# Optimization experiments

Measured on AMD Instinct MI355X. Metric: run time of the kernel, lower is better.

## Reference

```python
import jax, jax.numpy as jnp
import numpy as np


def _conv(x, w, b, pad):
    y = jax.lax.conv_general_dilated(
        x, w, window_strides=(1, 1), padding=[(pad, pad), (pad, pad)],
        dimension_numbers=('NCHW', 'OIHW', 'NCHW'))
    return y + b[None, :, None, None]


def _grid_sample(img, gxn, gyn):
    # img [N,C,H,W]; gxn,gyn [N,H,W] normalized coords.
    # Matches torch grid_sample(mode='bilinear', padding_mode='zeros', align_corners=False).
    N, C, H, W = img.shape
    ix = ((gxn + 1.0) * W - 1.0) * 0.5
    iy = ((gyn + 1.0) * H - 1.0) * 0.5
    ix0 = jnp.floor(ix); iy0 = jnp.floor(iy)
    ix1 = ix0 + 1.0; iy1 = iy0 + 1.0
    wx1 = ix - ix0; wy1 = iy - iy0
    wx0 = 1.0 - wx1; wy0 = 1.0 - wy1
    bidx = jnp.arange(N)[:, None, None]

    def gather(yy, xx):
        valid = (xx >= 0) & (xx < W) & (yy >= 0) & (yy < H)
        xc = jnp.clip(xx, 0, W - 1).astype(jnp.int32)
        yc = jnp.clip(yy, 0, H - 1).astype(jnp.int32)
        v = img[bidx, :, yc, xc]  # [N,H,W,C]
        return jnp.where(valid[..., None], v, jnp.zeros((), img.dtype))

    out = (gather(iy0, ix0) * (wy0 * wx0)[..., None]
           + gather(iy0, ix1) * (wy0 * wx1)[..., None]
           + gather(iy1, ix0) * (wy1 * wx0)[..., None]
           + gather(iy1, ix1) * (wy1 * wx1)[..., None])
    return jnp.transpose(out, (0, 3, 1, 2))  # [N,C,H,W]


def reference(inputs, state, i2h_w, i2h_b, i2f_w, i2f_b, h2f_w, h2f_b,
              flows_w, flows_b, wrap_w, wrap_b):
    B, T, Cin, H, W = inputs.shape
    hid = state.shape[1]
    L = flows_w.shape[0] // 2

    # input-to-hidden for all timesteps at once (as in the torch code)
    i2h = _conv(inputs.reshape(B * T, Cin, H, W), i2h_w, i2h_b, 1)
    i2h = i2h.reshape(B, T, 3 * hid, H, W)
    r_i, u_i, n_i = jnp.split(i2h, 3, axis=2)

    gx, gy = jnp.meshgrid(jnp.arange(W, dtype=inputs.dtype),
                          jnp.arange(H, dtype=inputs.dtype))  # each [H,W]

    def step(h, xs):
        x_t, r_t, u_t, n_t = xs
        f = jnp.tanh(_conv(x_t, i2f_w, i2f_b, 2) + _conv(h, h2f_w, h2f_b, 2))
        flows = _conv(f, flows_w, flows_b, 2).reshape(B, L, 2, H, W)
        # vgrid = grid + (-flow), then normalize by 2*v/size - 1
        vx = gx[None, None] - flows[:, :, 0]
        vy = gy[None, None] - flows[:, :, 1]
        gxn = 2.0 * vx / W - 1.0
        gyn = 2.0 * vy / H - 1.0
        img = jnp.broadcast_to(h[:, None], (B, L, hid, H, W)).reshape(B * L, hid, H, W)
        warped = _grid_sample(img, gxn.reshape(B * L, H, W), gyn.reshape(B * L, H, W))
        warped = warped.reshape(B, L * hid, H, W)
        h2h = _conv(warped, wrap_w, wrap_b, 0)
        r_h, u_h, n_h = jnp.split(h2h, 3, axis=1)
        r = jax.nn.sigmoid(r_t + r_h)
        u = jax.nn.sigmoid(u_t + u_h)
        n = jax.nn.sigmoid(n_t + r * n_h)  # note: sigmoid, faithful to source
        h_new = (1.0 - u) * n + u * h
        return h_new, h_new

    xs = (jnp.swapaxes(inputs, 0, 1),
          jnp.swapaxes(r_i, 0, 1),
          jnp.swapaxes(u_i, 0, 1),
          jnp.swapaxes(n_i, 0, 1))
    h_last, outs = jax.lax.scan(step, state, xs)
    outputs = jnp.swapaxes(outs, 0, 1)  # [B,T,hid,H,W]
    return outputs, h_last


def setup_inputs() -> dict:
    key = jax.random.key(0)
    ks = jax.random.split(key, 8)
    B, T, Cin, H, W = 4, 10, 8, 96, 96
    hid, L = 64, 13

    def w(k, shape):
        fan_in = int(np.prod(shape[1:]))
        return jax.random.normal(k, shape, jnp.float32) * (1.0 / np.sqrt(fan_in))

    return {
        'inputs': jax.random.normal(ks[0], (B, T, Cin, H, W), jnp.float32),
        'state': jnp.zeros((B, hid, H, W), jnp.float32),
        'i2h_w': w(ks[1], (3 * hid, Cin, 3, 3)), 'i2h_b': jnp.zeros((3 * hid,), jnp.float32),
        'i2f_w': w(ks[2], (32, Cin, 5, 5)), 'i2f_b': jnp.zeros((32,), jnp.float32),
        'h2f_w': w(ks[3], (32, hid, 5, 5)), 'h2f_b': jnp.zeros((32,), jnp.float32),
        'flows_w': w(ks[4], (2 * L, 32, 5, 5)), 'flows_b': jnp.zeros((2 * L,), jnp.float32),
        'wrap_w': w(ks[5], (3 * hid, hid * L, 1, 1)), 'wrap_b': jnp.zeros((3 * hid,), jnp.float32),
    }
```

## Files before the change

kernel.cpp:

```cpp
#include <hip/hip_runtime.h>
#include <math.h>

#define HW 9216

typedef __attribute__((ext_vector_type(8))) short short8;
typedef __attribute__((ext_vector_type(4))) short short4v;
typedef __attribute__((ext_vector_type(4))) float float4v;

__device__ __forceinline__ float sigmoidf_(float x) { return 1.0f / (1.0f + expf(-x)); }

__device__ __forceinline__ short bf16rne(float f) {
  unsigned u = __builtin_bit_cast(unsigned, f);
  unsigned r = (u + 0x7FFFu + ((u >> 16) & 1u)) >> 16;
  return (short)r;
}
__device__ __forceinline__ float bf2f(short s) {
  return __builtin_bit_cast(float, ((unsigned)(unsigned short)s) << 16);
}

__global__ __launch_bounds__(256) void k_wconv(const float* __restrict__ w,
                                               short* __restrict__ o)
{
  int i = blockIdx.x * 256 + threadIdx.x;
  if (i >= 192 * 832) return;
  int n = i / 832, k = i % 832;
  int l = k >> 6, c = k & 63;
  o[((size_t)l * 192 + n) * 64 + c] = bf16rne(w[i]);
}

__global__ __launch_bounds__(256) void k_pack(
    const float* __restrict__ wh, const float* __restrict__ wi,
    const float* __restrict__ flw, const float* __restrict__ wih,
    short* __restrict__ whK, short* __restrict__ wiK, short* __restrict__ flK,
    short* __restrict__ i2hK)
{
  int i = blockIdx.x * 256 + threadIdx.x;
  if (i < 51200) {
    int t = i / 2048, rem = i % 2048;
    int o = rem / 64, c = rem % 64;
    whK[i] = bf16rne(wh[((size_t)(o * 64 + c)) * 25 + t]);
  } else if (i < 58368) {
    int j = i - 51200;
    int g = j / 1024, rem = j % 1024;
    int o = rem / 32, k = rem % 32;
    int q = k / 8, ch = k % 8;
    int tap = g * 4 + q;
    wiK[j] = (tap < 25) ? bf16rne(wi[((size_t)(o * 8 + ch)) * 25 + tap]) : (short)0;
  } else if (i < 83968) {
    int j = i - 58368;
    int t = j / 1024, rem = j % 1024;
    int o = rem / 32, c = rem % 32;
    flK[j] = (o < 26) ? bf16rne(flw[((size_t)(o * 32 + c)) * 25 + t]) : (short)0;
  } else {
    int j = i - 83968;
    int g = j / 6144, rem = j % 6144;
    int n = rem / 32, k = rem % 32;
    int q = k / 8, ch = k % 8;
    int tap = g * 4 + q;
    i2hK[j] = (tap < 9) ? bf16rne(wih[((size_t)(n * 8 + ch)) * 9 + tap]) : (short)0;
  }
}

__global__ __launch_bounds__(256) void k_h2bf(const float* __restrict__ st,
                                              short* __restrict__ hbf)
{
  const int tid = threadIdx.x;
  const int pp = tid & 63, cg = tid >> 6;
  const int b = blockIdx.y;
  const int p = blockIdx.x * 64 + pp;
  short s[16];
  #pragma unroll
  for (int k = 0; k < 16; ++k)
    s[k] = bf16rne(st[((size_t)b * 64 + cg * 16 + k) * HW + p]);
  short* dst = hbf + ((size_t)b * HW + p) * 64 + cg * 16;
  *(short8*)dst = *(short8*)&s[0];
  *(short8*)(dst + 8) = *(short8*)&s[8];
}

__global__ __launch_bounds__(256) void k_x2bf(const float* __restrict__ inp,
                                              short* __restrict__ xbf)
{
  const int p  = blockIdx.x * 256 + threadIdx.x;
  const int bt = blockIdx.y;
  short s[8];
  #pragma unroll
  for (int ci = 0; ci < 8; ++ci)
    s[ci] = bf16rne(inp[((size_t)bt * 8 + ci) * HW + p]);
  *(short8*)(xbf + ((size_t)bt * HW + p) * 8) = *(short8*)s;
}

__global__ __launch_bounds__(256) void k_i2h(
    const short* __restrict__ xbf, int t_off,
    const short* __restrict__ wK, const float* __restrict__ bias,
    short* __restrict__ out)
{
  const int tid  = threadIdx.x;
  const int lane = tid & 63;
  const int w    = tid >> 6;
  const int ml = lane & 15, qd = lane >> 4;
  const int zz = blockIdx.y;
  const int t = (zz >> 2) + t_off, b = zz & 3;
  const int pw0 = blockIdx.x * 128 + w * 32;
  const short* xb = xbf + ((size_t)(b * 10 + t)) * HW * 8;

  short8 afr[2][3];
  #pragma unroll
  for (int s = 0; s < 2; ++s) {
    int px0 = pw0 + s * 16;
    int y0 = px0 / 96, xc0 = px0 % 96;
    #pragma unroll
    for (int g = 0; g < 3; ++g) {
      int tap = g * 4 + qd;
      int dy = tap / 3 - 1;
      int dx = tap % 3 - 1;
      int yy = y0 + dy, xx = xc0 + ml + dx;
      bool v = (tap < 9) && (yy >= 0) && (yy < 96) && (xx >= 0) && (xx < 96);
      short8 a = {};
      if (v) a = *(const short8*)(xb + (size_t)(px0 + ml + dy * 96 + dx) * 8);
      afr[s][g] = a;
    }
  }

  float4v acc[2][12];
  #pragma unroll
  for (int s = 0; s < 2; ++s)
    #pragma unroll
    for (int j = 0; j < 12; ++j)
      #pragma unroll
      for (int r = 0; r < 4; ++r) acc[s][j][r] = 0.0f;

  #pragma unroll
  for (int j = 0; j < 12; ++j) {
    #pragma unroll
    for (int g = 0; g < 3; ++g) {
      short8 bf = *(const short8*)(wK + ((size_t)(g * 192 + j * 16 + ml)) * 32 + qd * 8);
      acc[0][j] = __builtin_amdgcn_mfma_f32_16x16x32_bf16(afr[0][g], bf, acc[0][j], 0, 0, 0);
      acc[1][j] = __builtin_amdgcn_mfma_f32_16x16x32_bf16(afr[1][g], bf, acc[1][j], 0, 0, 0);
    }
  }

  #pragma unroll
  for (int j = 0; j < 12; ++j) {
    float bv = bias[j * 16 + ml];
    #pragma unroll
    for (int s = 0; s < 2; ++s) {
      short4v o4;
      #pragma unroll
      for (int r = 0; r < 4; ++r) o4[r] = bf16rne(acc[s][j][r] + bv);
      *(short4v*)(out + ((size_t)(zz * 192 + j * 16 + ml)) * HW
                      + pw0 + s * 16 + qd * 4) = o4;
    }
  }
}

__global__ __launch_bounds__(256) void k_f(
    const short* __restrict__ xbf, int t,
    const short* __restrict__ hbf,
    const short* __restrict__ whK,
    const short* __restrict__ wiK,
    const float* __restrict__ bi, const float* __restrict__ bh,
    short* __restrict__ fbf)
{
  const int tid = threadIdx.x;
  const int lane = tid & 63;
  const int w = tid >> 6;
  const int ml = lane & 15, qd = lane >> 4;
  const int b = blockIdx.y;
  const int px0 = blockIdx.x * 64 + w * 16;
  const int y0 = px0 / 96, xc0 = px0 % 96;
  const int xcol = xc0 + ml;
  const int px = px0 + ml;
  const short* hb = hbf + (size_t)b * HW * 64;
  const short* xb = xbf + ((size_t)(b * 10 + t)) * HW * 8;

  float4v acc0 = {0.f, 0.f, 0.f, 0.f};
  float4v acc1 = {0.f, 0.f, 0.f, 0.f};

  #pragma unroll
  for (int ky = 0; ky < 5; ++ky) {
    int yy = y0 + ky - 2;
    if (yy < 0 || yy >= 96) continue;
    #pragma unroll
    for (int kx = 0; kx < 5; ++kx) {
      int xx = xcol + kx - 2;
      bool cv = (xx >= 0) && (xx < 96);
      int off = (ky - 2) * 96 + (kx - 2);
      const short* ap = hb + (size_t)(px + off) * 64 + qd * 8;
      short8 a0 = {}, a1 = {};
      if (cv) { a0 = *(const short8*)ap; a1 = *(const short8*)(ap + 32); }
      int tap = ky * 5 + kx;
      const short* bp = whK + ((size_t)tap * 32 + ml) * 64 + qd * 8;
      short8 b00 = *(const short8*)bp;
      short8 b01 = *(const short8*)(bp + 32);
      short8 b10 = *(const short8*)(bp + 16 * 64);
      short8 b11 = *(const short8*)(bp + 16 * 64 + 32);
      acc0 = __builtin_amdgcn_mfma_f32_16x16x32_bf16(a0, b00, acc0, 0, 0, 0);
      acc0 = __builtin_amdgcn_mfma_f32_16x16x32_bf16(a1, b01, acc0, 0, 0, 0);
      acc1 = __builtin_amdgcn_mfma_f32_16x16x32_bf16(a0, b10, acc1, 0, 0, 0);
      acc1 = __builtin_amdgcn_mfma_f32_16x16x32_bf16(a1, b11, acc1, 0, 0, 0);
    }
  }

  #pragma unroll
  for (int g = 0; g < 7; ++g) {
    int tap = g * 4 + qd;
    int dy = tap / 5 - 2;
    int dx = tap - (dy + 2) * 5 - 2;
    int yy = y0 + dy, xx = xcol + dx;
    bool v = (tap < 25) && (yy >= 0) && (yy < 96) && (xx >= 0) && (xx < 96);
    short8 a = {};
    if (v) a = *(const short8*)(xb + (size_t)(px + dy * 96 + dx) * 8);
    const short* bp = wiK + ((size_t)g * 32 + ml) * 32 + qd * 8;
    short8 b0 = *(const short8*)bp;
    short8 b1 = *(const short8*)(bp + 16 * 32);
    acc0 = __builtin_amdgcn_mfma_f32_16x16x32_bf16(a, b0, acc0, 0, 0, 0);
    acc1 = __builtin_amdgcn_mfma_f32_16x16x32_bf16(a, b1, acc1, 0, 0, 0);
  }

  short* fo = fbf + (size_t)b * HW * 32;
  #pragma unroll
  for (int i = 0; i < 2; ++i) {
    int o = i * 16 + ml;
    float bias = bi[o] + bh[o];
    float4v a = i ? acc1 : acc0;
    #pragma unroll
    for (int r = 0; r < 4; ++r) {
      int p2 = px0 + qd * 4 + r;
      fo[(size_t)p2 * 32 + o] = bf16rne(tanhf(a[r] + bias));
    }
  }
}

__global__ __launch_bounds__(256) void k_flows(
    const short* __restrict__ fbf,
    const short* __restrict__ flK,
    const float* __restrict__ bias,
    float* __restrict__ fls)
{
  const int tid = threadIdx.x;
  const int lane = tid & 63;
  const int w = tid >> 6;
  const int ml = lane & 15, qd = lane >> 4;
  const int b = blockIdx.y;
  const int px0 = blockIdx.x * 64 + w * 16;
  const int y0 = px0 / 96, xc0 = px0 % 96;
  const int xcol = xc0 + ml;
  const int px = px0 + ml;
  const short* fb = fbf + (size_t)b * HW * 32;

  float4v acc0 = {0.f, 0.f, 0.f, 0.f};
  float4v acc1 = {0.f, 0.f, 0.f, 0.f};

  #pragma unroll
  for (int ky = 0; ky < 5; ++ky) {
    int yy = y0 + ky - 2;
    if (yy < 0 || yy >= 96) continue;
    #pragma unroll
    for (int kx = 0; kx < 5; ++kx) {
      int xx = xcol + kx - 2;
      bool cv = (xx >= 0) && (xx < 96);
      int off = (ky - 2) * 96 + (kx - 2);
      short8 a = {};
      if (cv) a = *(const short8*)(fb + (size_t)(px + off) * 32 + qd * 8);
      int tap = ky * 5 + kx;
      const short* bp = flK + ((size_t)tap * 32 + ml) * 32 + qd * 8;
      short8 b0 = *(const short8*)bp;
      short8 b1 = *(const short8*)(bp + 16 * 32);
      acc0 = __builtin_amdgcn_mfma_f32_16x16x32_bf16(a, b0, acc0, 0, 0, 0);
      acc1 = __builtin_amdgcn_mfma_f32_16x16x32_bf16(a, b1, acc1, 0, 0, 0);
    }
  }

  float* fo = fls + (size_t)b * 26 * HW;
  #pragma unroll
  for (int i = 0; i < 2; ++i) {
    int o = i * 16 + ml;
    if (o < 26) {
      float bv = bias[o];
      float4v a = i ? acc1 : acc0;
      #pragma unroll
      for (int r = 0; r < 4; ++r)
        fo[(size_t)o * HW + px0 + qd * 4 + r] = a[r] + bv;
    }
  }
}

__global__ __launch_bounds__(256) void k_fused(
    const float* __restrict__ fls,
    const float* __restrict__ hbase, long long hstr,
    const short* __restrict__ hbf_in,
    const short* __restrict__ i2h,
    const short* __restrict__ wbf,
    const float* __restrict__ wb,
    float* __restrict__ outb, long long ostr,
    short* __restrict__ hbf_out,
    float* __restrict__ lastb)
{
  __shared__ __align__(16) char smem_raw[49920];
  short* lds_w = (short*)smem_raw;
  short* lds_v = lds_w + 192 * 72;
  float* lds_h = (float*)smem_raw;
  short* hpack = (short*)smem_raw;

  const int tid = threadIdx.x;
  const int pp  = tid & 63;
  const int cg  = tid >> 6;
  const int ii  = blockIdx.x;
  const int xcd = ii & 7;
  const int b   = xcd >> 1;
  const int tile = ((ii >> 3) << 1) | (xcd & 1);
  const int p   = tile * 64 + pp;
  const int ypix = p / 96, xpix = p % 96;
  const float* hb  = hbase + (size_t)b * hstr;
  const short* hvp = hbf_in + ((size_t)b * HW) * 64 + cg * 16;
  const float* flb = fls + (size_t)b * 26 * HW;
  const int ml = pp & 15;
  const int qd = pp >> 4;

  float4v acc[3][4];
  #pragma unroll
  for (int i = 0; i < 3; ++i)
    #pragma unroll
    for (int j = 0; j < 4; ++j)
      #pragma unroll
      for (int r = 0; r < 4; ++r) acc[i][j][r] = 0.0f;

  for (int l = 0; l < 13; ++l) {
    __syncthreads();
    {
      const short* wsrc = wbf + (size_t)l * 192 * 64;
      #pragma unroll
      for (int it = 0; it < 6; ++it) {
        int idx = tid + it * 256;
        int n = idx >> 3, c8 = (idx & 7) * 8;
        short8 v = *(const short8*)(wsrc + n * 64 + c8);
        *(short8*)(lds_w + n * 72 + c8) = v;
      }
    }
    float fx = flb[(size_t)(2 * l) * HW + p];
    float fy = flb[(size_t)(2 * l + 1) * HW + p];
    float vx = (float)xpix - fx;
    float vy = (float)ypix - fy;
    float gxn = 2.0f * vx / 96.0f - 1.0f;
    float gyn = 2.0f * vy / 96.0f - 1.0f;
    float ix = ((gxn + 1.0f) * 96.0f - 1.0f) * 0.5f;
    float iy = ((gyn + 1.0f) * 96.0f - 1.0f) * 0.5f;
    float x0f = floorf(ix), y0f = floorf(iy);
    float wx1 = ix - x0f, wy1 = iy - y0f;
    float wx0 = 1.0f - wx1, wy0 = 1.0f - wy1;
    int x0 = (int)x0f, y0 = (int)y0f;
    bool vx0 = (x0 >= 0) && (x0 < 96);
    bool vx1 = (x0 + 1 >= 0) && (x0 + 1 < 96);
    bool vy0g = (y0 >= 0) && (y0 < 96);
    bool vy1g = (y0 + 1 >= 0) && (y0 + 1 < 96);
    int o00 = (vx0 && vy0g) ? (y0 * 96 + x0)           : -1;
    int o01 = (vx1 && vy0g) ? (y0 * 96 + x0 + 1)       : -1;
    int o10 = (vx0 && vy1g) ? ((y0 + 1) * 96 + x0)     : -1;
    int o11 = (vx1 && vy1g) ? ((y0 + 1) * 96 + x0 + 1) : -1;
    float w00 = wy0 * wx0, w01 = wy0 * wx1, w10 = wy1 * wx0, w11 = wy1 * wx1;

    float sum[16];
    #pragma unroll
    for (int k = 0; k < 16; ++k) sum[k] = 0.0f;
    #define TAP_(off, wgt)                                            \
      if ((off) >= 0) {                                               \
        const short* tp = hvp + (size_t)(off) * 64;                   \
        short8 u0 = *(const short8*)tp;                               \
        short8 u1 = *(const short8*)(tp + 8);                         \
        _Pragma("unroll")                                             \
        for (int k = 0; k < 8; ++k) {                                 \
          sum[k]     += (wgt) * bf2f(u0[k]);                          \
          sum[k + 8] += (wgt) * bf2f(u1[k]);                          \
        }                                                             \
      }
    TAP_(o00, w00) TAP_(o01, w01) TAP_(o10, w10) TAP_(o11, w11)
    #undef TAP_
    short vv[16];
    #pragma unroll
    for (int k = 0; k < 16; ++k) vv[k] = bf16rne(sum[k]);
    *(short8*)(lds_v + pp * 72 + cg * 16)     = *(short8*)&vv[0];
    *(short8*)(lds_v + pp * 72 + cg * 16 + 8) = *(short8*)&vv[8];
    __syncthreads();

    #pragma unroll
    for (int ks = 0; ks < 2; ++ks) {
      short8 af[3], bfr[4];
      #pragma unroll
      for (int i = 0; i < 3; ++i)
        af[i] = *(const short8*)(lds_w + (48 * cg + i * 16 + ml) * 72 + ks * 32 + qd * 8);
      #pragma unroll
      for (int j = 0; j < 4; ++j)
        bfr[j] = *(const short8*)(lds_v + (j * 16 + ml) * 72 + ks * 32 + qd * 8);
      #pragma unroll
      for (int i = 0; i < 3; ++i)
        #pragma unroll
        for (int j = 0; j < 4; ++j)
          acc[i][j] = __builtin_amdgcn_mfma_f32_16x16x32_bf16(af[i], bfr[j], acc[i][j], 0, 0, 0);
    }
  }

  __syncthreads();
  #pragma unroll
  for (int i = 0; i < 3; ++i)
    #pragma unroll
    for (int j = 0; j < 4; ++j)
      #pragma unroll
      for (int r = 0; r < 4; ++r) {
        int ch = 48 * cg + i * 16 + qd * 4 + r;
        int px = j * 16 + ml;
        lds_h[ch * 65 + px] = acc[i][j][r];
      }
  __syncthreads();

  const short* i2hb = i2h + (size_t)b * 192 * HW + p;
  float* ob = outb + (size_t)b * ostr;
  float hnv[16];
  #pragma unroll
  for (int k = 0; k < 16; ++k) {
    int cch = cg + k * 4;
    float rh = lds_h[cch * 65 + pp] + wb[cch];
    float uh = lds_h[(64 + cch) * 65 + pp] + wb[64 + cch];
    float nh = lds_h[(128 + cch) * 65 + pp] + wb[128 + cch];
    float rt = bf2f(i2hb[(size_t)cch * HW]);
    float ut = bf2f(i2hb[(size_t)(64 + cch) * HW]);
    float nt = bf2f(i2hb[(size_t)(128 + cch) * HW]);
    float rr = sigmoidf_(rt + rh);
    float uu = sigmoidf_(ut + uh);
    float nn = sigmoidf_(nt + rr * nh);
    float hp = hb[(size_t)cch * HW + p];
    float hn = (1.0f - uu) * nn + uu * hp;
    ob[(size_t)cch * HW + p] = hn;
    if (lastb) lastb[((size_t)b * 64 + cch) * HW + p] = hn;
    hnv[k] = hn;
  }

  __syncthreads();
  #pragma unroll
  for (int k = 0; k < 16; ++k)
    hpack[pp * 80 + cg + 4 * k] = bf16rne(hnv[k]);
  __syncthreads();
  {
    int px = tid >> 2, g = tid & 3;
    short8 a0 = *(short8*)(hpack + px * 80 + g * 16);
    short8 a1 = *(short8*)(hpack + px * 80 + g * 16 + 8);
    short* dst = hbf_out + ((size_t)b * HW + tile * 64 + px) * 64 + g * 16;
    *(short8*)dst = a0;
    *(short8*)(dst + 8) = a1;
  }
}

extern "C" void kernel_launch(void* const* d_in, const int* in_sizes, int n_in,
                              void* d_out, int out_size, void* d_ws, size_t ws_size,
                              hipStream_t stream)
{
  const float* inp   = (const float*)d_in[0];
  const float* state = (const float*)d_in[1];
  const float* i2h_w = (const float*)d_in[2];
  const float* i2h_b = (const float*)d_in[3];
  const float* i2f_w = (const float*)d_in[4];
  const float* i2f_b = (const float*)d_in[5];
  const float* h2f_w = (const float*)d_in[6];
  const float* h2f_b = (const float*)d_in[7];
  const float* fl_w  = (const float*)d_in[8];
  const float* fl_b  = (const float*)d_in[9];
  const float* wr_w  = (const float*)d_in[10];
  const float* wr_b  = (const float*)d_in[11];
  float* out = (float*)d_out;
  float* ws  = (float*)d_ws;

  const long long F_I2HB1 = 3538944;
  const long long F_FBF   = 589824;
  const long long F_FLS   = 958464;
  const long long F_HB    = 1179648;
  const long long F_XBF   = 1474560;
  const long long F_WBF   = 79872;
  const long long F_WHK   = 25600;
  const long long F_WIK   = 3584;
  const long long F_FLK   = 12800;
  const long long F_I2HK  = 9216;
  const long long OB      = (long long)10 * 64 * HW;

  const long long fixed = F_FBF + F_FLS + 2 * F_HB + F_XBF + F_WBF
                        + F_WHK + F_WIK + F_FLK + F_I2HK;
  bool batched = ws_size >= (size_t)(10 * F_I2HB1 + fixed) * 4ULL;
  long long i2h_fl = batched ? 10 * F_I2HB1 : F_I2HB1;

  short* ws_i2h = (short*)ws;
  float* fwp    = ws + i2h_fl;
  float* ws_fbf_f = fwp;              fwp += F_FBF;
  float* ws_fls   = fwp;              fwp += F_FLS;
  float* hbfA_f   = fwp;              fwp += F_HB;
  float* hbfB_f   = fwp;              fwp += F_HB;
  float* xbf_f    = fwp;              fwp += F_XBF;
  float* wbf_f    = fwp;              fwp += F_WBF;
  float* whK_f    = fwp;              fwp += F_WHK;
  float* wiK_f    = fwp;              fwp += F_WIK;
  float* flK_f    = fwp;              fwp += F_FLK;
  float* i2hK_f   = fwp;
  short* ws_fbf  = (short*)ws_fbf_f;
  short* hbfA    = (short*)hbfA_f;
  short* hbfB    = (short*)hbfB_f;
  short* ws_xbf  = (short*)xbf_f;
  short* ws_wbf  = (short*)wbf_f;
  short* ws_whK  = (short*)whK_f;
  short* ws_wiK  = (short*)wiK_f;
  short* ws_flK  = (short*)flK_f;
  short* ws_i2hK = (short*)i2hK_f;

  k_wconv<<<dim3(624), 256, 0, stream>>>(wr_w, ws_wbf);
  k_pack<<<dim3(400), 256, 0, stream>>>(h2f_w, i2f_w, fl_w, i2h_w,
                                        ws_whK, ws_wiK, ws_flK, ws_i2hK);
  k_h2bf<<<dim3(144, 4), 256, 0, stream>>>(state, hbfA);
  k_x2bf<<<dim3(36, 40), 256, 0, stream>>>(inp, ws_xbf);
  if (batched)
    k_i2h<<<dim3(72, 40), 256, 0, stream>>>(ws_xbf, 0, ws_i2hK, i2h_b, ws_i2h);

  for (int t = 0; t < 10; ++t) {
    const float* hbase = (t == 0) ? state : (out + (size_t)(t - 1) * 64 * HW);
    long long hstr = (t == 0) ? (long long)64 * HW : OB;
    short* hin  = (t & 1) ? hbfB : hbfA;
    short* hout = (t & 1) ? hbfA : hbfB;

    if (!batched)
      k_i2h<<<dim3(72, 4), 256, 0, stream>>>(ws_xbf, t, ws_i2hK, i2h_b, ws_i2h);
    k_f<<<dim3(144, 4), 256, 0, stream>>>(ws_xbf, t, hin, ws_whK, ws_wiK,
                                          i2f_b, h2f_b, ws_fbf);
    k_flows<<<dim3(144, 4), 256, 0, stream>>>(ws_fbf, ws_flK, fl_b, ws_fls);

    const short* i2h_t = batched ? (ws_i2h + (size_t)t * 2 * F_I2HB1) : ws_i2h;
    float* outbase = out + (size_t)t * 64 * HW;
    float* lastb = (t == 9) ? (out + (size_t)4 * 10 * 64 * HW) : nullptr;
    k_fused<<<dim3(576), 256, 0, stream>>>(ws_fls, hbase, hstr, hin, i2h_t,
                                           ws_wbf, wr_b, outbase, OB, hout, lastb);
  }
}
```

Baseline: 1.515 ms.

## Software-pipeline warp gather and weight loads; stage flows in LDS; coalesce i2h stores

The fused warp/GEMM kernel now prefetches the next level's weight tile and the bilinear gather taps into registers while the current level's MFMAs run. This overlaps global-memory latency with compute. All 26 flow channels for the tile are staged into LDS once up front. The kernel also sets a min-blocks-per-CU hint of 3. Separately, the i2h kernel stages its outputs through LDS so the global stores are wide and contiguous, at the cost of a large LDS allocation and extra register pressure.

```diff
diff --git a/kernel.cpp b/kernel.cpp
--- a/kernel.cpp
+++ b/kernel.cpp
@@ -94,6 +94,7 @@
     const short* __restrict__ wK, const float* __restrict__ bias,
     short* __restrict__ out)
 {
+  __shared__ __align__(16) short lds_o[192 * 136];
   const int tid  = threadIdx.x;
   const int lane = tid & 63;
   const int w    = tid >> 6;
@@ -147,9 +148,16 @@
       short4v o4;
       #pragma unroll
       for (int r = 0; r < 4; ++r) o4[r] = bf16rne(acc[s][j][r] + bv);
-      *(short4v*)(out + ((size_t)(zz * 192 + j * 16 + ml)) * HW
-                      + pw0 + s * 16 + qd * 4) = o4;
-    }
+      *(short4v*)(lds_o + (j * 16 + ml) * 136 + w * 32 + s * 16 + qd * 4) = o4;
+    }
+  }
+  __syncthreads();
+  const int pblk = blockIdx.x * 128;
+  #pragma unroll
+  for (int k = 0; k < 12; ++k) {
+    int r = (tid >> 4) + k * 16;
+    short8 vvv = *(short8*)(lds_o + r * 136 + (tid & 15) * 8);
+    *(short8*)(out + ((size_t)(zz * 192 + r)) * HW + pblk + (tid & 15) * 8) = vvv;
   }
 }
 
@@ -285,7 +293,7 @@
   }
 }
 
-__global__ __launch_bounds__(256) void k_fused(
+__global__ __launch_bounds__(256, 3) void k_fused(
     const float* __restrict__ fls,
     const float* __restrict__ hbase, long long hstr,
     const short* __restrict__ hbf_in,
@@ -299,6 +307,7 @@
   __shared__ __align__(16) char smem_raw[49920];
   short* lds_w = (short*)smem_raw;
   short* lds_v = lds_w + 192 * 72;
+  float* lds_f = (float*)(smem_raw + 36864);
   float* lds_h = (float*)smem_raw;
   short* hpack = (short*)smem_raw;
 
@@ -317,6 +326,15 @@
   const int ml = pp & 15;
   const int qd = pp >> 4;
 
+  #pragma unroll
+  for (int it = 0; it < 7; ++it) {
+    int idx = it * 256 + tid;
+    if (idx < 1664) {
+      int c = idx >> 6, pp2 = idx & 63;
+      lds_f[pp2 * 26 + c] = flb[(size_t)c * HW + tile * 64 + pp2];
+    }
+  }
+
   float4v acc[3][4];
   #pragma unroll
   for (int i = 0; i < 3; ++i)
@@ -325,20 +343,15 @@
       #pragma unroll
       for (int r = 0; r < 4; ++r) acc[i][j][r] = 0.0f;
 
-  for (int l = 0; l < 13; ++l) {
-    __syncthreads();
-    {
-      const short* wsrc = wbf + (size_t)l * 192 * 64;
-      #pragma unroll
-      for (int it = 0; it < 6; ++it) {
-        int idx = tid + it * 256;
-        int n = idx >> 3, c8 = (idx & 7) * 8;
-        short8 v = *(const short8*)(wsrc + n * 64 + c8);
-        *(short8*)(lds_w + n * 72 + c8) = v;
-      }
-    }
-    float fx = flb[(size_t)(2 * l) * HW + p];
-    float fy = flb[(size_t)(2 * l + 1) * HW + p];
+  int   o_[4];
+  float wt_[4];
+  short8 u_[4][2];
+  short8 wreg[6];
+  short vv[16];
+
+  auto comp_offs = [&](int l) {
+    float fx = lds_f[pp * 26 + 2 * l];
+    float fy = lds_f[pp * 26 + 2 * l + 1];
     float vx = (float)xpix - fx;
     float vy = (float)ypix - fy;
     float gxn = 2.0f * vx / 96.0f - 1.0f;
@@ -353,35 +366,71 @@
     bool vx1 = (x0 + 1 >= 0) && (x0 + 1 < 96);
     bool vy0g = (y0 >= 0) && (y0 < 96);
     bool vy1g = (y0 + 1 >= 0) && (y0 + 1 < 96);
-    int o00 = (vx0 && vy0g) ? (y0 * 96 + x0)           : -1;
-    int o01 = (vx1 && vy0g) ? (y0 * 96 + x0 + 1)       : -1;
-    int o10 = (vx0 && vy1g) ? ((y0 + 1) * 96 + x0)     : -1;
-    int o11 = (vx1 && vy1g) ? ((y0 + 1) * 96 + x0 + 1) : -1;
-    float w00 = wy0 * wx0, w01 = wy0 * wx1, w10 = wy1 * wx0, w11 = wy1 * wx1;
-
+    o_[0] = (vx0 && vy0g) ? (y0 * 96 + x0)           : -1;
+    o_[1] = (vx1 && vy0g) ? (y0 * 96 + x0 + 1)       : -1;
+    o_[2] = (vx0 && vy1g) ? ((y0 + 1) * 96 + x0)     : -1;
+    o_[3] = (vx1 && vy1g) ? ((y0 + 1) * 96 + x0 + 1) : -1;
+    wt_[0] = wy0 * wx0; wt_[1] = wy0 * wx1; wt_[2] = wy1 * wx0; wt_[3] = wy1 * wx1;
+  };
+  auto load_gather = [&]() {
+    #pragma unroll
+    for (int q = 0; q < 4; ++q) {
+      short8 z = {};
+      u_[q][0] = z; u_[q][1] = z;
+      if (o_[q] >= 0) {
+        const short* tp = hvp + (size_t)o_[q] * 64;
+        u_[q][0] = *(const short8*)tp;
+        u_[q][1] = *(const short8*)(tp + 8);
+      }
+    }
+  };
+  auto load_w = [&](int l) {
+    const short* wsrc = wbf + (size_t)l * 192 * 64;
+    #pragma unroll
+    for (int it = 0; it < 6; ++it) {
+      int idx = tid + it * 256;
+      int n = idx >> 3, c8 = (idx & 7) * 8;
+      wreg[it] = *(const short8*)(wsrc + n * 64 + c8);
+    }
+  };
+  auto comp_vv = [&]() {
     float sum[16];
     #pragma unroll
     for (int k = 0; k < 16; ++k) sum[k] = 0.0f;
-    #define TAP_(off, wgt)                                            \
-      if ((off) >= 0) {                                               \
-        const short* tp = hvp + (size_t)(off) * 64;                   \
-        short8 u0 = *(const short8*)tp;                               \
-        short8 u1 = *(const short8*)(tp + 8);                         \
-        _Pragma("unroll")                                             \
-        for (int k = 0; k < 8; ++k) {                                 \
-          sum[k]     += (wgt) * bf2f(u0[k]);                          \
-          sum[k + 8] += (wgt) * bf2f(u1[k]);                          \
-        }                                                             \
+    #pragma unroll
+    for (int q = 0; q < 4; ++q) {
+      #pragma unroll
+      for (int k = 0; k < 8; ++k) {
+        sum[k]     += wt_[q] * bf2f(u_[q][0][k]);
+        sum[k + 8] += wt_[q] * bf2f(u_[q][1][k]);
       }
-    TAP_(o00, w00) TAP_(o01, w01) TAP_(o10, w10) TAP_(o11, w11)
-    #undef TAP_
-    short vv[16];
+    }
     #pragma unroll
     for (int k = 0; k < 16; ++k) vv[k] = bf16rne(sum[k]);
+  };
+
+  __syncthreads();
+  load_w(0);
+  comp_offs(0);
+  load_gather();
+  comp_vv();
+
+  for (int l = 0; l < 13; ++l) {
+    __syncthreads();
+    #pragma unroll
+    for (int it = 0; it < 6; ++it) {
+      int idx = tid + it * 256;
+      int n = idx >> 3, c8 = (idx & 7) * 8;
+      *(short8*)(lds_w + n * 72 + c8) = wreg[it];
+    }
     *(short8*)(lds_v + pp * 72 + cg * 16)     = *(short8*)&vv[0];
     *(short8*)(lds_v + pp * 72 + cg * 16 + 8) = *(short8*)&vv[8];
     __syncthreads();
-
+    if (l < 12) {
+      load_w(l + 1);
+      comp_offs(l + 1);
+      load_gather();
+    }
     #pragma unroll
     for (int ks = 0; ks < 2; ++ks) {
       short8 af[3], bfr[4];
@@ -397,6 +446,7 @@
         for (int j = 0; j < 4; ++j)
           acc[i][j] = __builtin_amdgcn_mfma_f32_16x16x32_bf16(af[i], bfr[j], acc[i][j], 0, 0, 0);
     }
+    if (l < 12) comp_vv();
   }
 
   __syncthreads();
```

Result: no change. 1.495 ms (-1.3%).
